# Performance work log

Hardware: AMD Instinct MI355X
Metric: run time of the kernel (lower is better)

The kernel has to match this reference:

```python
import jax, jax.numpy as jnp
import numpy as np

EMB = 1024
HEADS = 16
HEAD_DIM = EMB // HEADS
HIDDEN = 4 * EMB
SEQ = 2048
BATCH = 4


def setup_inputs() -> dict:
    key = jax.random.key(0)
    ks = jax.random.split(key, 16)
    s = 0.02
    return {
        "x": jax.random.normal(ks[0], (BATCH, SEQ, EMB), jnp.float32),
        "ln1_scale": jnp.ones((EMB,), jnp.float32),
        "ln1_shift": jnp.zeros((EMB,), jnp.float32),
        "ln2_scale": jnp.ones((EMB,), jnp.float32),
        "ln2_shift": jnp.zeros((EMB,), jnp.float32),
        # weights stored [in, out]; y = x @ W + b (equivalent to torch Linear)
        "W_q": jax.random.normal(ks[1], (EMB, EMB), jnp.float32) * s,
        "W_k": jax.random.normal(ks[2], (EMB, EMB), jnp.float32) * s,
        "W_v": jax.random.normal(ks[3], (EMB, EMB), jnp.float32) * s,
        "W_o": jax.random.normal(ks[4], (EMB, EMB), jnp.float32) * s,
        "b_o": jnp.zeros((EMB,), jnp.float32),
        "W_fc": jax.random.normal(ks[5], (EMB, HIDDEN), jnp.float32) * s,
        "b_fc": jnp.zeros((HIDDEN,), jnp.float32),
        "W_proj": jax.random.normal(ks[6], (HIDDEN, EMB), jnp.float32) * s,
        "b_proj": jnp.zeros((EMB,), jnp.float32),
    }


def _layernorm(x, scale, shift, eps=1e-5):
    mean = jnp.mean(x, axis=-1, keepdims=True)
    var = jnp.mean(jnp.square(x - mean), axis=-1, keepdims=True)  # unbiased=False
    return scale * (x - mean) / jnp.sqrt(var + eps) + shift


def _gelu(x):
    c = jnp.sqrt(jnp.asarray(2.0 / jnp.pi, x.dtype))
    return 0.5 * x * (1.0 + jnp.tanh(c * (x + 0.044715 * x ** 3)))


def _attention(x, W_q, W_k, W_v, W_o, b_o):
    b, s, _ = x.shape
    q = (x @ W_q).reshape(b, s, HEADS, HEAD_DIM)
    k = (x @ W_k).reshape(b, s, HEADS, HEAD_DIM)
    v = (x @ W_v).reshape(b, s, HEADS, HEAD_DIM)
    scores = jnp.einsum("bqhd,bkhd->bhqk", q, k)
    causal = jnp.tril(jnp.ones((s, s), bool))  # keep lower-triangular
    scores = jnp.where(causal, scores, -jnp.inf)
    w = jax.nn.softmax(scores / jnp.sqrt(jnp.asarray(HEAD_DIM, x.dtype)), axis=-1)
    ctx = jnp.einsum("bhqk,bkhd->bqhd", w, v).reshape(b, s, EMB)
    return ctx @ W_o + b_o


def reference(x, ln1_scale, ln1_shift, ln2_scale, ln2_shift,
              W_q, W_k, W_v, W_o, b_o, W_fc, b_fc, W_proj, b_proj):
    h = x + _attention(_layernorm(x, ln1_scale, ln1_shift), W_q, W_k, W_v, W_o, b_o)
    m = _layernorm(h, ln2_scale, ln2_shift)
    m = _gelu(m @ W_fc + b_fc) @ W_proj + b_proj
    return h + m
```

## Files before the change

kernel.cpp:

```cpp
#include <hip/hip_runtime.h>

typedef __attribute__((ext_vector_type(8))) short bf16x8;
typedef __attribute__((ext_vector_type(2))) unsigned uint2v;
typedef __attribute__((ext_vector_type(4))) float f32x4;

#define MFMA_BF16(a, b, c) __builtin_amdgcn_mfma_f32_16x16x32_bf16((a), (b), (c), 0, 0, 0)
#define VMCNT(N) asm volatile("s_waitcnt vmcnt(" #N ")" ::: "memory")
#define BAR() asm volatile("s_barrier" ::: "memory")

__device__ __forceinline__ unsigned short bf16rn(float f) {
  unsigned u = __builtin_bit_cast(unsigned, f);
  u += 0x7fffu + ((u >> 16) & 1u);
  return (unsigned short)(u >> 16);
}

__device__ __forceinline__ void gld_lds16(const void* g, void* l) {
  __builtin_amdgcn_global_load_lds((const __attribute__((address_space(1))) void*)g,
                                   (__attribute__((address_space(3))) void*)l, 16, 0, 0);
}

__global__ __launch_bounds__(256) void convT_kernel(
    const float* __restrict__ wq, const float* __restrict__ wk,
    const float* __restrict__ wv, const float* __restrict__ wo,
    const float* __restrict__ wfc, const float* __restrict__ wpj,
    unsigned short* __restrict__ wsb)
{
  const int bid = blockIdx.x;
  const float* src; unsigned short* dst; int K, N, lb;
  if (bid < 1024) {
    const int m = bid >> 8; lb = bid & 255; K = 1024; N = 1024;
    src = (m == 0) ? wq : (m == 1) ? wk : (m == 2) ? wv : wo;
    dst = wsb + (size_t)m * 1048576u;
  } else if (bid < 2048) {
    lb = bid - 1024; K = 1024; N = 4096; src = wfc; dst = wsb + 4194304u;
  } else {
    lb = bid - 2048; K = 4096; N = 1024; src = wpj; dst = wsb + 8388608u;
  }
  const int tiles_k = K >> 6;
  const int tk = lb % tiles_k, tn = lb / tiles_k;
  const int k0 = tk << 6, n0 = tn << 6;
  const int t = threadIdx.x, kq = t & 15, nq = t >> 4;
  float4 r[4];
#pragma unroll
  for (int i = 0; i < 4; ++i)
    r[i] = *(const float4*)(src + (size_t)(k0 + kq * 4 + i) * N + n0 + nq * 4);
#pragma unroll
  for (int j = 0; j < 4; ++j) {
    ushort4 o;
    o.x = bf16rn(((const float*)&r[0])[j]);
    o.y = bf16rn(((const float*)&r[1])[j]);
    o.z = bf16rn(((const float*)&r[2])[j]);
    o.w = bf16rn(((const float*)&r[3])[j]);
    *(ushort4*)(dst + (size_t)(n0 + nq * 4 + j) * K + k0 + kq * 4) = o;
  }
}

__global__ __launch_bounds__(256) void ln_kernel(
    const float* __restrict__ x, const float* __restrict__ sc,
    const float* __restrict__ sh, unsigned short* __restrict__ out)
{
  const int row = blockIdx.x, t = threadIdx.x;
  const float4 v = *(const float4*)(x + (size_t)row * 1024 + t * 4);
  float s = v.x + v.y + v.z + v.w;
  float q = v.x * v.x + v.y * v.y + v.z * v.z + v.w * v.w;
#pragma unroll
  for (int off = 1; off < 64; off <<= 1) { s += __shfl_xor(s, off); q += __shfl_xor(q, off); }
  __shared__ float ps[4], pq[4];
  if ((t & 63) == 0) { ps[t >> 6] = s; pq[t >> 6] = q; }
  __syncthreads();
  s = ps[0] + ps[1] + ps[2] + ps[3];
  q = pq[0] + pq[1] + pq[2] + pq[3];
  const float mean = s * (1.f / 1024.f);
  const float var = q * (1.f / 1024.f) - mean * mean;
  const float inv = rsqrtf(var + 1e-5f);
  const float4 scv = *(const float4*)(sc + t * 4);
  const float4 shv = *(const float4*)(sh + t * 4);
  ushort4 o;
  o.x = bf16rn((v.x - mean) * inv * scv.x + shv.x);
  o.y = bf16rn((v.y - mean) * inv * scv.y + shv.y);
  o.z = bf16rn((v.z - mean) * inv * scv.z + shv.z);
  o.w = bf16rn((v.w - mean) * inv * scv.w + shv.w);
  *(ushort4*)(out + (size_t)row * 1024 + t * 4) = o;
}

template<int EPI>
__global__ __launch_bounds__(256) void gemm_bt(
    const unsigned short* __restrict__ A, const unsigned short* __restrict__ Bt,
    int M, int N, int K,
    unsigned short* __restrict__ outb, float* __restrict__ outf,
    const float* __restrict__ bias, const float* __restrict__ resid)
{
  __shared__ char smem[36864];
  const int t = threadIdx.x;
  const int lane = t & 63, w = t >> 6;
  const int g = lane >> 4, l15 = lane & 15;
  const int wr = w >> 1, wc = w & 1;
  const int bid = blockIdx.x;
  const int j = bid >> 3;
  const int tm = (bid & 7) * 8 + (j & 7);
  const int tn = j >> 3;
  const int m0 = tm * 128, n0 = tn * 128;

  f32x4 acc[4][4] = {};

  const int nkt = K >> 5;
  for (int kt = 0; kt < nkt; ++kt) {
    const int k0 = kt << 5;
    __syncthreads();
#pragma unroll
    for (int it = 0; it < 2; ++it) {
      const int c = it * 256 + t;
      const int row = c >> 2;
      const int ce = (c & 3) << 3;
      gld_lds16(A + (size_t)(m0 + row) * K + k0 + ce,
                smem + ((it * 256 + w * 64) << 4));
      gld_lds16(Bt + (size_t)(n0 + row) * K + k0 + ce,
                smem + 8192 + ((it * 256 + w * 64) << 4));
    }
    __syncthreads();
    bf16x8 a[4], b[4];
#pragma unroll
    for (int mi = 0; mi < 4; ++mi)
      a[mi] = *(const bf16x8*)(smem + (wr * 64 + mi * 16 + l15) * 64 + g * 16);
#pragma unroll
    for (int ni = 0; ni < 4; ++ni)
      b[ni] = *(const bf16x8*)(smem + 8192 + (wc * 64 + ni * 16 + l15) * 64 + g * 16);
#pragma unroll
    for (int mi = 0; mi < 4; ++mi)
#pragma unroll
      for (int ni = 0; ni < 4; ++ni)
        acc[mi][ni] = MFMA_BF16(a[mi], b[ni], acc[mi][ni]);
  }

  if constexpr (EPI == 1) {
    __syncthreads();
    unsigned short* T = (unsigned short*)(smem + w * 9216);
#pragma unroll
    for (int mi = 0; mi < 4; ++mi)
#pragma unroll
      for (int ni = 0; ni < 4; ++ni)
#pragma unroll
        for (int r = 0; r < 4; ++r)
          T[(ni * 16 + l15) * 72 + mi * 16 + 4 * g + r] = bf16rn(acc[mi][ni][r]);
    asm volatile("s_waitcnt lgkmcnt(0)" ::: "memory");
    const int bidx = m0 >> 11;
    const int srow = (m0 & 2047) + wr * 64 + ((lane & 7) << 3);
#pragma unroll
    for (int rr = 0; rr < 8; ++rr) {
      const int trow = rr * 8 + (lane >> 3);
      bf16x8 v = *(const bf16x8*)((char*)T + trow * 144 + ((lane & 7) << 4));
      *(bf16x8*)(outb + (size_t)(bidx * 1024 + n0 + wc * 64 + trow) * 2048 + srow) = v;
    }
  }
}

template<int EPI>
__global__ __launch_bounds__(256, 2) void g128(
    const unsigned short* __restrict__ A, const unsigned short* __restrict__ Bt,
    int N, int K,
    unsigned short* __restrict__ outb, float* __restrict__ outf,
    const float* __restrict__ bias, const float* __restrict__ resid)
{
  extern __shared__ char smem[];
  constexpr int BUFSZ = 32768;
  const int t = threadIdx.x, lane = t & 63, w = t >> 6;
  const int g = lane >> 4, l15 = lane & 15;
  const int wr = w >> 1, wc = w & 1;
  const int bid = blockIdx.x;
  const int tm = (bid & 7) * 8 + ((bid >> 3) & 7);
  const int tn = bid >> 6;
  const int m0 = tm << 7, n0 = tn << 7;

  const int srow = t >> 3;
  const int colswz = (((t & 7) ^ (srow & 7)) << 3);
  const unsigned short* pA = A + (size_t)(m0 + srow) * K + colswz;
  const unsigned short* pB = Bt + (size_t)(n0 + srow) * K + colswz;
  const int ldw = w << 10;

  auto stA = [&](int TT, char* buf) {
#pragma unroll
    for (int i = 0; i < 4; ++i)
      gld_lds16(pA + TT * 64 + (size_t)(i * 32) * K, buf + i * 4096 + ldw);
  };
  auto stB02 = [&](int TT, char* buf) {
    gld_lds16(pB + TT * 64, buf + 16384 + ldw);
    gld_lds16(pB + TT * 64 + (size_t)64 * K, buf + 16384 + 8192 + ldw);
  };
  auto stB13 = [&](int TT, char* buf) {
    gld_lds16(pB + TT * 64 + (size_t)32 * K, buf + 16384 + 4096 + ldw);
    gld_lds16(pB + TT * 64 + (size_t)96 * K, buf + 16384 + 12288 + ldw);
  };

  const int sw0 = (((0 + g) ^ (l15 & 7)) << 4);
  const int sw1 = (((4 + g) ^ (l15 & 7)) << 4);
  const int NT = K >> 6;

  f32x4 acc[4][4] = {};
  bf16x8 av[4][2], bv0[2][2], bv1[2][2];

#define LDA_ALL(CB) { _Pragma("unroll") for (int mi = 0; mi < 4; ++mi) {                  \
    const int row_ = (wr * 64 + mi * 16 + l15) * 128;                                     \
    av[mi][0] = *(const bf16x8*)((CB) + row_ + sw0);                                      \
    av[mi][1] = *(const bf16x8*)((CB) + row_ + sw1); } }
#define LDB_H(CB, H, BV) { _Pragma("unroll") for (int ni = 0; ni < 2; ++ni) {             \
    const int row_ = 16384 + (wc * 64 + (H) * 32 + ni * 16 + l15) * 128;                  \
    BV[ni][0] = *(const bf16x8*)((CB) + row_ + sw0);                                      \
    BV[ni][1] = *(const bf16x8*)((CB) + row_ + sw1); } }
#define MMH(BV, H) { __builtin_amdgcn_s_setprio(1);                                       \
    _Pragma("unroll") for (int mi = 0; mi < 4; ++mi)                                      \
      _Pragma("unroll") for (int ni = 0; ni < 2; ++ni) {                                  \
        acc[mi][(H)*2+ni] = MFMA_BF16(av[mi][0], BV[ni][0], acc[mi][(H)*2+ni]);           \
        acc[mi][(H)*2+ni] = MFMA_BF16(av[mi][1], BV[ni][1], acc[mi][(H)*2+ni]);  }        \
    __builtin_amdgcn_s_setprio(0); }

  stA(0, smem); stB02(0, smem); stB13(0, smem);
  stA(1, smem + BUFSZ); stB02(1, smem + BUFSZ);
  VMCNT(6);
  BAR();

  for (int kt = 0; kt < NT; ++kt) {
    char* cb = smem + (kt & 1) * BUFSZ;
    char* ob = smem + ((kt & 1) ^ 1) * BUFSZ;
    LDA_ALL(cb);
    LDB_H(cb, 0, bv0);
    if (kt + 1 < NT) stB13(kt + 1, ob);
    BAR();
    MMH(bv0, 0);
    BAR();
    LDB_H(cb, 1, bv1);
    if (kt + 2 < NT) { stA(kt + 2, cb); stB02(kt + 2, cb); VMCNT(6); }
    else if (kt + 1 < NT) VMCNT(0);
    BAR();
    MMH(bv1, 1);
    BAR();
  }
#undef LDA_ALL
#undef LDB_H
#undef MMH

  if constexpr (EPI == 2) {
#pragma unroll
    for (int mi = 0; mi < 4; ++mi) {
      const int ro = mi * 16 + g * 4;
#pragma unroll
      for (int ci = 0; ci < 4; ++ci) {
        const int n = n0 + wc * 64 + ci * 16 + l15;
        const float bn = bias[n];
#pragma unroll
        for (int r = 0; r < 4; ++r) {
          const size_t m = m0 + wr * 64 + ro + r;
          outf[m * N + n] = acc[mi][ci][r] + bn + resid[m * N + n];
        }
      }
    }
  } else {
    __syncthreads();
    char* wsl = smem + w * 8192;
#pragma unroll
    for (int mi = 0; mi < 4; ++mi) {
      const int ro = mi * 16 + g * 4;
#pragma unroll
      for (int ci = 0; ci < 4; ++ci) {
        const int co = ci * 16 + l15;
        float bn = 0.f;
        if constexpr (EPI == 3) bn = bias[n0 + wc * 64 + co];
#pragma unroll
        for (int r = 0; r < 4; ++r) {
          float v = acc[mi][ci][r];
          if constexpr (EPI == 3) {
            v += bn;
            const float inner = v + 0.044715f * v * v * v;
            const float s = exp2f(-2.3022085f * inner);
            v = v / (1.0f + s);
          }
          *(unsigned short*)(wsl + (ro + r) * 128 + co * 2) = bf16rn(v);
        }
      }
    }
#pragma unroll
    for (int s = 0; s < 8; ++s) {
      const int row = s * 8 + (lane >> 3);
      bf16x8 vv = *(const bf16x8*)(wsl + row * 128 + (lane & 7) * 16);
      *(bf16x8*)(outb + (size_t)(m0 + wr * 64 + row) * N + n0 + wc * 64 + (lane & 7) * 8) = vv;
    }
  }
}

__global__ __launch_bounds__(256) void attn_kernel(
    const unsigned short* __restrict__ qg, const unsigned short* __restrict__ kg,
    const unsigned short* __restrict__ vT, unsigned short* __restrict__ ctx)
{
  __shared__ char smem[34816];
  const int bh = blockIdx.x, b = bh >> 4, h = bh & 15;
  const int t = threadIdx.x, lane = t & 63, w = t >> 6, g = lane >> 4, l15 = lane & 15;
  char* Ks = smem;
  char* Vs = smem + 8192;
  char* Pt = smem + 16384 + w * 4608;

  const float SC = 0.18033688011112042f;

  const int qt = 15 - (int)blockIdx.y;
  const int q0 = qt << 7;
  const int q0w = q0 + w * 32;

  bf16x8 qf[2][2];
#pragma unroll
  for (int mi = 0; mi < 2; ++mi)
#pragma unroll
    for (int ks = 0; ks < 2; ++ks)
      qf[mi][ks] = *(const bf16x8*)(qg + (size_t)(b * 2048 + q0w + mi * 16 + l15) * 2048 +
                                    h * 64 + ks * 32 + g * 8);

  f32x4 acc[2][4] = {};
  float lsum[2][4] = {};

  const int ntile = 2 * qt + 2;
  for (int kt = 0; kt < ntile; ++kt) {
    const int kv0 = kt << 6;
    __syncthreads();
#pragma unroll
    for (int it = 0; it < 2; ++it) {
      const int c = it * 256 + t;
      const int row = c >> 3;
      const int wb = (c & 7) << 4;
      const int sw = (wb ^ ((row & 7) << 4)) >> 1;
      gld_lds16(kg + (size_t)(b * 2048 + kv0 + row) * 2048 + h * 64 + sw,
                Ks + ((it * 256 + w * 64) << 4));
      gld_lds16(vT + (size_t)(b * 1024 + h * 64 + row) * 2048 + kv0 + sw,
                Vs + ((it * 256 + w * 64) << 4));
    }
    __syncthreads();

    f32x4 sf[2][4] = {};
#pragma unroll
    for (int nb = 0; nb < 4; ++nb) {
      const int krow = nb * 16 + l15;
#pragma unroll
      for (int ks = 0; ks < 2; ++ks) {
        bf16x8 kf = *(const bf16x8*)(Ks + krow * 128 +
                                     (((ks * 32 + g * 8) << 1) ^ ((krow & 7) << 4)));
        sf[0][nb] = MFMA_BF16(qf[0][ks], kf, sf[0][nb]);
        sf[1][nb] = MFMA_BF16(qf[1][ks], kf, sf[1][nb]);
      }
    }
    if (kv0 + 63 > q0w) {
#pragma unroll
      for (int mi = 0; mi < 2; ++mi)
#pragma unroll
        for (int nb = 0; nb < 4; ++nb)
#pragma unroll
          for (int r = 0; r < 4; ++r) {
            const int qq = q0w + mi * 16 + 4 * g + r;
            const int kk = kv0 + nb * 16 + l15;
            if (kk > qq) sf[mi][nb][r] = -__builtin_inff();
          }
    }
#pragma unroll
    for (int mi = 0; mi < 2; ++mi)
#pragma unroll
      for (int nb = 0; nb < 4; ++nb)
#pragma unroll
        for (int r = 0; r < 4; ++r) {
          const float p = exp2f(__builtin_fmaf(sf[mi][nb][r], SC, -4.0f));
          sf[mi][nb][r] = p;
          lsum[mi][r] += p;
        }
#pragma unroll
    for (int mi = 0; mi < 2; ++mi)
#pragma unroll
      for (int nb = 0; nb < 4; ++nb) {
        uint2v dw;
        asm("v_cvt_pk_bf16_f32 %0, %1, %2"
            : "=v"(dw.x) : "v"(sf[mi][nb][0]), "v"(sf[mi][nb][1]));
        asm("v_cvt_pk_bf16_f32 %0, %1, %2"
            : "=v"(dw.y) : "v"(sf[mi][nb][2]), "v"(sf[mi][nb][3]));
        *(uint2v*)(Pt + (nb * 16 + l15) * 72 + ((mi * 16 + 4 * g) << 1)) = dw;
      }
    asm volatile("s_waitcnt lgkmcnt(0)" ::: "memory");
#pragma unroll
    for (int mi = 0; mi < 2; ++mi)
#pragma unroll
      for (int ks = 0; ks < 2; ++ks) {
        const char* pp = Pt + (ks * 32 + g * 8) * 72 + ((mi * 16 + l15) << 1);
        bf16x8 pa;
#pragma unroll
        for (int jj = 0; jj < 8; ++jj)
          pa[jj] = *(const short*)(pp + jj * 72);
#pragma unroll
        for (int nb = 0; nb < 4; ++nb) {
          const int drow = nb * 16 + l15;
          bf16x8 vb = *(const bf16x8*)(Vs + drow * 128 +
                                       (((ks * 32 + g * 8) << 1) ^ ((drow & 7) << 4)));
          acc[mi][nb] = MFMA_BF16(pa, vb, acc[mi][nb]);
        }
      }
  }
#pragma unroll
  for (int mi = 0; mi < 2; ++mi)
#pragma unroll
    for (int r = 0; r < 4; ++r) {
      float s = lsum[mi][r];
      s += __shfl_xor(s, 1);
      s += __shfl_xor(s, 2);
      s += __shfl_xor(s, 4);
      s += __shfl_xor(s, 8);
      lsum[mi][r] = s;
    }
#pragma unroll
  for (int mi = 0; mi < 2; ++mi) {
    float inv[4];
#pragma unroll
    for (int r = 0; r < 4; ++r) inv[r] = 1.0f / lsum[mi][r];
#pragma unroll
    for (int nb = 0; nb < 4; ++nb)
#pragma unroll
      for (int r = 0; r < 4; ++r)
        ctx[(size_t)(b * 2048 + q0w + mi * 16 + 4 * g + r) * 1024 + h * 64 + nb * 16 + l15] =
            bf16rn(acc[mi][nb][r] * inv[r]);
  }
}

extern "C" void kernel_launch(void* const* d_in, const int* in_sizes, int n_in,
                              void* d_out, int out_size, void* d_ws, size_t ws_size,
                              hipStream_t stream)
{
  const float* x   = (const float*)d_in[0];
  const float* l1s = (const float*)d_in[1];
  const float* l1b = (const float*)d_in[2];
  const float* l2s = (const float*)d_in[3];
  const float* l2b = (const float*)d_in[4];
  const float* Wq  = (const float*)d_in[5];
  const float* Wk  = (const float*)d_in[6];
  const float* Wv  = (const float*)d_in[7];
  const float* Wo  = (const float*)d_in[8];
  const float* bo  = (const float*)d_in[9];
  const float* Wfc = (const float*)d_in[10];
  const float* bfc = (const float*)d_in[11];
  const float* Wpj = (const float*)d_in[12];
  const float* bpj = (const float*)d_in[13];
  float* out = (float*)d_out;
  char* ws = (char*)d_ws;

  unsigned short* wT   = (unsigned short*)ws;
  unsigned short* wqkT = wT;
  unsigned short* wvT  = wT + 2097152u;
  unsigned short* woT  = wT + 3145728u;
  unsigned short* wfcT = wT + 4194304u;
  unsigned short* wpjT = wT + 8388608u;
  unsigned short* ln1x = (unsigned short*)(ws + 25165824u);
  unsigned short* qkb  = (unsigned short*)(ws + 41943040u);
  unsigned short* vTb  = (unsigned short*)(ws + 75497472u);
  unsigned short* ctx  = (unsigned short*)(ws + 92274688u);
  unsigned short* ln2x = ctx;
  float* hbuf          = (float*)(ws + 109051904u);
  unsigned short* fcb  = (unsigned short*)(ws + 25165824u);

  convT_kernel<<<3072, 256, 0, stream>>>(Wq, Wk, Wv, Wo, Wfc, Wpj, wT);
  ln_kernel<<<8192, 256, 0, stream>>>(x, l1s, l1b, ln1x);
  g128<0><<<1024, 256, 65536, stream>>>(ln1x, wqkT, 2048, 1024,
                                        qkb, nullptr, nullptr, nullptr);
  gemm_bt<1><<<512, 256, 0, stream>>>(ln1x, wvT, 8192, 1024, 1024,
                                      vTb, nullptr, nullptr, nullptr);
  attn_kernel<<<dim3(64, 16), 256, 0, stream>>>(qkb, qkb + 1024, vTb, ctx);
  g128<2><<<512, 256, 65536, stream>>>(ctx, woT, 1024, 1024,
                                       nullptr, hbuf, bo, x);
  ln_kernel<<<8192, 256, 0, stream>>>(hbuf, l2s, l2b, ln2x);
  g128<3><<<2048, 256, 65536, stream>>>(ln2x, wfcT, 4096, 1024,
                                        fcb, nullptr, bfc, nullptr);
  g128<2><<<512, 256, 65536, stream>>>(fcb, wpjT, 1024, 4096,
                                       nullptr, out, bpj, hbuf);
}
```

Before: 366.1 us.

## Pair causal query tiles per block and use 8 waves of 16 rows each

```diff
diff --git a/kernel.cpp b/kernel.cpp
--- a/kernel.cpp
+++ b/kernel.cpp
@@ -286,137 +286,119 @@
   }
 }
 
-__global__ __launch_bounds__(256) void attn_kernel(
+__global__ __launch_bounds__(512) void attn_kernel(
     const unsigned short* __restrict__ qg, const unsigned short* __restrict__ kg,
     const unsigned short* __restrict__ vT, unsigned short* __restrict__ ctx)
 {
-  __shared__ char smem[34816];
+  __shared__ char smem[36864];
   const int bh = blockIdx.x, b = bh >> 4, h = bh & 15;
   const int t = threadIdx.x, lane = t & 63, w = t >> 6, g = lane >> 4, l15 = lane & 15;
   char* Ks = smem;
   char* Vs = smem + 8192;
-  char* Pt = smem + 16384 + w * 4608;
+  char* Pt = smem + 16384 + w * 2560;
 
   const float SC = 0.18033688011112042f;
 
-  const int qt = 15 - (int)blockIdx.y;
-  const int q0 = qt << 7;
-  const int q0w = q0 + w * 32;
-
-  bf16x8 qf[2][2];
-#pragma unroll
-  for (int mi = 0; mi < 2; ++mi)
+  const int srow = t >> 3;
+  const int ssw = ((((t & 7) << 4) ^ ((srow & 7) << 4)) >> 1);
+
+  for (int pass = 0; pass < 2; ++pass) {
+    const int qt = pass ? 15 - (int)blockIdx.y : (int)blockIdx.y;
+    const int q0 = qt << 7;
+    const int q0w = q0 + w * 16;
+
+    bf16x8 qf[2];
 #pragma unroll
     for (int ks = 0; ks < 2; ++ks)
-      qf[mi][ks] = *(const bf16x8*)(qg + (size_t)(b * 2048 + q0w + mi * 16 + l15) * 2048 +
-                                    h * 64 + ks * 32 + g * 8);
-
-  f32x4 acc[2][4] = {};
-  float lsum[2][4] = {};
-
-  const int ntile = 2 * qt + 2;
-  for (int kt = 0; kt < ntile; ++kt) {
-    const int kv0 = kt << 6;
-    __syncthreads();
-#pragma unroll
-    for (int it = 0; it < 2; ++it) {
-      const int c = it * 256 + t;
-      const int row = c >> 3;
-      const int wb = (c & 7) << 4;
-      const int sw = (wb ^ ((row & 7) << 4)) >> 1;
-      gld_lds16(kg + (size_t)(b * 2048 + kv0 + row) * 2048 + h * 64 + sw,
-                Ks + ((it * 256 + w * 64) << 4));
-      gld_lds16(vT + (size_t)(b * 1024 + h * 64 + row) * 2048 + kv0 + sw,
-                Vs + ((it * 256 + w * 64) << 4));
-    }
-    __syncthreads();
-
-    f32x4 sf[2][4] = {};
-#pragma unroll
-    for (int nb = 0; nb < 4; ++nb) {
-      const int krow = nb * 16 + l15;
-#pragma unroll
-      for (int ks = 0; ks < 2; ++ks) {
-        bf16x8 kf = *(const bf16x8*)(Ks + krow * 128 +
-                                     (((ks * 32 + g * 8) << 1) ^ ((krow & 7) << 4)));
-        sf[0][nb] = MFMA_BF16(qf[0][ks], kf, sf[0][nb]);
-        sf[1][nb] = MFMA_BF16(qf[1][ks], kf, sf[1][nb]);
-      }
-    }
-    if (kv0 + 63 > q0w) {
-#pragma unroll
-      for (int mi = 0; mi < 2; ++mi)
+      qf[ks] = *(const bf16x8*)(qg + (size_t)(b * 2048 + q0w + l15) * 2048 +
+                                h * 64 + ks * 32 + g * 8);
+
+    f32x4 acc[4] = {};
+    float lsum[4] = {};
+
+    const int ntile = 2 * qt + 2;
+    for (int kt = 0; kt < ntile; ++kt) {
+      const int kv0 = kt << 6;
+      __syncthreads();
+      gld_lds16(kg + (size_t)(b * 2048 + kv0 + srow) * 2048 + h * 64 + ssw,
+                Ks + ((t >> 3) << 7));
+      gld_lds16(vT + (size_t)(b * 1024 + h * 64 + srow) * 2048 + kv0 + ssw,
+                Vs + ((t >> 3) << 7));
+      __syncthreads();
+
+      f32x4 sf[4] = {};
+#pragma unroll
+      for (int nb = 0; nb < 4; ++nb) {
+        const int krow = nb * 16 + l15;
+#pragma unroll
+        for (int ks = 0; ks < 2; ++ks) {
+          bf16x8 kf = *(const bf16x8*)(Ks + krow * 128 +
+                                       (((ks * 32 + g * 8) << 1) ^ ((krow & 7) << 4)));
+          sf[nb] = MFMA_BF16(qf[ks], kf, sf[nb]);
+        }
+      }
+      if (kv0 + 63 > q0w) {
 #pragma unroll
         for (int nb = 0; nb < 4; ++nb)
 #pragma unroll
           for (int r = 0; r < 4; ++r) {
-            const int qq = q0w + mi * 16 + 4 * g + r;
+            const int qq = q0w + 4 * g + r;
             const int kk = kv0 + nb * 16 + l15;
-            if (kk > qq) sf[mi][nb][r] = -__builtin_inff();
+            if (kk > qq) sf[nb][r] = -__builtin_inff();
           }
-    }
-#pragma unroll
-    for (int mi = 0; mi < 2; ++mi)
+      }
 #pragma unroll
       for (int nb = 0; nb < 4; ++nb)
 #pragma unroll
         for (int r = 0; r < 4; ++r) {
-          const float p = exp2f(__builtin_fmaf(sf[mi][nb][r], SC, -4.0f));
-          sf[mi][nb][r] = p;
-          lsum[mi][r] += p;
+          const float p = exp2f(__builtin_fmaf(sf[nb][r], SC, -4.0f));
+          sf[nb][r] = p;
+          lsum[r] += p;
         }
-#pragma unroll
-    for (int mi = 0; mi < 2; ++mi)
 #pragma unroll
       for (int nb = 0; nb < 4; ++nb) {
         uint2v dw;
         asm("v_cvt_pk_bf16_f32 %0, %1, %2"
-            : "=v"(dw.x) : "v"(sf[mi][nb][0]), "v"(sf[mi][nb][1]));
+            : "=v"(dw.x) : "v"(sf[nb][0]), "v"(sf[nb][1]));
         asm("v_cvt_pk_bf16_f32 %0, %1, %2"
-            : "=v"(dw.y) : "v"(sf[mi][nb][2]), "v"(sf[mi][nb][3]));
-        *(uint2v*)(Pt + (nb * 16 + l15) * 72 + ((mi * 16 + 4 * g) << 1)) = dw;
-      }
-    asm volatile("s_waitcnt lgkmcnt(0)" ::: "memory");
-#pragma unroll
-    for (int mi = 0; mi < 2; ++mi)
+            : "=v"(dw.y) : "v"(sf[nb][2]), "v"(sf[nb][3]));
+        *(uint2v*)(Pt + (nb * 16 + l15) * 40 + (g << 3)) = dw;
+      }
+      asm volatile("s_waitcnt lgkmcnt(0)" ::: "memory");
 #pragma unroll
       for (int ks = 0; ks < 2; ++ks) {
-        const char* pp = Pt + (ks * 32 + g * 8) * 72 + ((mi * 16 + l15) << 1);
+        const char* pp = Pt + (ks * 32 + g * 8) * 40 + (l15 << 1);
         bf16x8 pa;
 #pragma unroll
         for (int jj = 0; jj < 8; ++jj)
-          pa[jj] = *(const short*)(pp + jj * 72);
+          pa[jj] = *(const short*)(pp + jj * 40);
 #pragma unroll
         for (int nb = 0; nb < 4; ++nb) {
           const int drow = nb * 16 + l15;
           bf16x8 vb = *(const bf16x8*)(Vs + drow * 128 +
                                        (((ks * 32 + g * 8) << 1) ^ ((drow & 7) << 4)));
-          acc[mi][nb] = MFMA_BF16(pa, vb, acc[mi][nb]);
+          acc[nb] = MFMA_BF16(pa, vb, acc[nb]);
         }
       }
-  }
-#pragma unroll
-  for (int mi = 0; mi < 2; ++mi)
+    }
 #pragma unroll
     for (int r = 0; r < 4; ++r) {
-      float s = lsum[mi][r];
+      float s = lsum[r];
       s += __shfl_xor(s, 1);
       s += __shfl_xor(s, 2);
       s += __shfl_xor(s, 4);
       s += __shfl_xor(s, 8);
-      lsum[mi][r] = s;
-    }
-#pragma unroll
-  for (int mi = 0; mi < 2; ++mi) {
+      lsum[r] = s;
+    }
     float inv[4];
 #pragma unroll
-    for (int r = 0; r < 4; ++r) inv[r] = 1.0f / lsum[mi][r];
+    for (int r = 0; r < 4; ++r) inv[r] = 1.0f / lsum[r];
 #pragma unroll
     for (int nb = 0; nb < 4; ++nb)
 #pragma unroll
       for (int r = 0; r < 4; ++r)
-        ctx[(size_t)(b * 2048 + q0w + mi * 16 + 4 * g + r) * 1024 + h * 64 + nb * 16 + l15] =
-            bf16rn(acc[mi][nb][r] * inv[r]);
+        ctx[(size_t)(b * 2048 + q0w + 4 * g + r) * 1024 + h * 64 + nb * 16 + l15] =
+            bf16rn(acc[nb][r] * inv[r]);
   }
 }
 
@@ -461,7 +443,7 @@
                                         qkb, nullptr, nullptr, nullptr);
   gemm_bt<1><<<512, 256, 0, stream>>>(ln1x, wvT, 8192, 1024, 1024,
                                       vTb, nullptr, nullptr, nullptr);
-  attn_kernel<<<dim3(64, 16), 256, 0, stream>>>(qkb, qkb + 1024, vTb, ctx);
+  attn_kernel<<<dim3(64, 8), 512, 0, stream>>>(qkb, qkb + 1024, vTb, ctx);
   g128<2><<<512, 256, 65536, stream>>>(ctx, woT, 1024, 1024,
                                        nullptr, hbuf, bo, x);
   ln_kernel<<<8192, 256, 0, stream>>>(hbuf, l2s, l2b, ln2x);
```

After: 346.2 us. 5.4% less time.
